# Performance work log

Hardware: AMD Instinct MI355X
Metric: run time of the kernel (lower is better)

The kernel has to match this reference:

```python
import jax, jax.numpy as jnp
import numpy as np

B, C, H, W = 32, 256, 64, 64
MIP, OUP = 8, 256
BN_EPS = 1e-5


def setup_inputs() -> dict:
    key = jax.random.key(0)
    ks = jax.random.split(key, 8)
    x = jax.random.normal(ks[0], (B, C, H, W), dtype=jnp.float32)
    # 1x1 conv weights stored as (out_ch, in_ch); BN in eval mode (running stats)
    w1 = jax.random.normal(ks[1], (MIP, C), dtype=jnp.float32) * 0.05
    bn_gamma = jnp.ones((MIP,), jnp.float32)
    bn_beta = jnp.zeros((MIP,), jnp.float32)
    bn_mean = jax.random.normal(ks[2], (MIP,), dtype=jnp.float32) * 0.1
    bn_var = jax.random.uniform(ks[3], (MIP,), dtype=jnp.float32) + 0.5
    wh = jax.random.normal(ks[4], (OUP, MIP), dtype=jnp.float32) * 0.1
    ww = jax.random.normal(ks[5], (OUP, MIP), dtype=jnp.float32) * 0.1
    return {"x": x, "w1": w1, "bn_gamma": bn_gamma, "bn_beta": bn_beta,
            "bn_mean": bn_mean, "bn_var": bn_var, "wh": wh, "ww": ww}


def _hswish(y):
    return y * jnp.clip(y + 3.0, 0.0, 6.0) / 6.0


def reference(x, w1, bn_gamma, bn_beta, bn_mean, bn_var, wh, ww):
    b, c, h, w = x.shape
    identity = x
    # Shift (mode='max'): pooled softmax profiles, outer product bias map
    bias_h = jax.nn.softmax(jnp.max(x, axis=3, keepdims=True), axis=2)  # (b,c,h,1)
    bias_w = jax.nn.softmax(jnp.max(x, axis=2, keepdims=True), axis=3)  # (b,c,1,w)
    xb = x + bias_h * bias_w  # outer product via broadcast == matmul((h,1),(1,w))
    # avg-pool profiles, concat along spatial axis -> (b,c,h+w,1)
    a_h = jnp.mean(xb, axis=3, keepdims=True)                 # (b,c,h,1)
    a_w = jnp.mean(xb, axis=2, keepdims=True).transpose(0, 1, 3, 2)  # (b,c,w,1)
    y = jnp.concatenate([a_h, a_w], axis=2)                   # (b,c,h+w,1)
    # 1x1 conv -> BN (eval) -> h_swish
    y = jnp.einsum('mc,bcsl->bmsl', w1, y)
    scale = (bn_gamma / jnp.sqrt(bn_var + BN_EPS)).reshape(1, -1, 1, 1)
    shift = (bn_beta - bn_mean * bn_gamma / jnp.sqrt(bn_var + BN_EPS)).reshape(1, -1, 1, 1)
    y = _hswish(y * scale + shift)
    # split, 1x1 convs, sigmoid gates
    y_h, y_w = y[:, :, :h], y[:, :, h:]
    g_h = jax.nn.sigmoid(jnp.einsum('om,bmhl->bohl', wh, y_h))               # (b,oup,h,1)
    g_w = jax.nn.sigmoid(jnp.einsum('om,bmwl->bowl', ww, y_w)).transpose(0, 1, 3, 2)  # (b,oup,1,w)
    return identity * g_w * g_h
```

## Files before the change

kernel.cpp:

```cpp
#include <hip/hip_runtime.h>
#include <math.h>

#define Bn 32
#define Cn 256
#define Hn 64
#define Wn 64
#define MIP 8
#define OUP 256
#define BN_EPS 1e-5f

__global__ __launch_bounds__(256) void stats_kernel(const float* __restrict__ x,
                                                    float* __restrict__ A) {
    const int bc = blockIdx.x;
    const float* xp = x + (size_t)bc * (Hn * Wn);
    __shared__ float tile[Hn * 65];
    const int t = threadIdx.x;

#pragma unroll
    for (int k = 0; k < 4; ++k) {
        int i4  = t + 256 * k;
        int idx = i4 * 4;
        int h = idx >> 6;
        int w = idx & 63;
        float4 v = ((const float4*)xp)[i4];
        float* dst = &tile[h * 65 + w];
        dst[0] = v.x; dst[1] = v.y; dst[2] = v.z; dst[3] = v.w;
    }
    __syncthreads();

    float red_max = -INFINITY, red_sum = 0.f;
    if (t < 64) {
        int h = t;
#pragma unroll 8
        for (int w = 0; w < Wn; ++w) {
            float v = tile[h * 65 + w];
            red_max = fmaxf(red_max, v);
            red_sum += v;
        }
    } else if (t < 128) {
        int w = t - 64;
#pragma unroll 8
        for (int h = 0; h < Hn; ++h) {
            float v = tile[h * 65 + w];
            red_max = fmaxf(red_max, v);
            red_sum += v;
        }
    }

    if (t < 128) {
        float m = red_max;
#pragma unroll
        for (int off = 32; off > 0; off >>= 1) m = fmaxf(m, __shfl_xor(m, off));
        float e = expf(red_max - m);
        float se = e;
#pragma unroll
        for (int off = 32; off > 0; off >>= 1) se += __shfl_xor(se, off);
        float bias = e / se;
        float a = red_sum * (1.0f / 64.0f) + bias * (1.0f / 64.0f);
        A[(size_t)bc * 128 + t] = a;
    }
}

__global__ __launch_bounds__(256) void gates_kernel(const float* __restrict__ A,
                                                    const float* __restrict__ w1,
                                                    const float* __restrict__ bn_gamma,
                                                    const float* __restrict__ bn_beta,
                                                    const float* __restrict__ bn_mean,
                                                    const float* __restrict__ bn_var,
                                                    const float* __restrict__ wh,
                                                    const float* __restrict__ ww,
                                                    float* __restrict__ G) {
    const int b = blockIdx.x;
    const int t = threadIdx.x;
    const int s  = t & 127;
    const int mb = t >> 7;

    const float* Ab = A + (size_t)b * Cn * 128;

    float acc[4] = {0.f, 0.f, 0.f, 0.f};
    for (int c = 0; c < Cn; ++c) {
        float a = Ab[(size_t)c * 128 + s];
#pragma unroll
        for (int k = 0; k < 4; ++k)
            acc[k] += w1[(mb + 2 * k) * Cn + c] * a;
    }

    __shared__ float yact[MIP][128];
#pragma unroll
    for (int k = 0; k < 4; ++k) {
        int m = mb + 2 * k;
        float sc = bn_gamma[m] * rsqrtf(bn_var[m] + BN_EPS);
        float sh = bn_beta[m] - bn_mean[m] * sc;
        float v = acc[k] * sc + sh;
        v = v * fminf(fmaxf(v + 3.0f, 0.0f), 6.0f) * (1.0f / 6.0f);
        yact[m][s] = v;
    }
    __syncthreads();

    float ym[MIP];
#pragma unroll
    for (int m = 0; m < MIP; ++m) ym[m] = yact[m][s];
    const float* w2 = (s < 64) ? wh : ww;

    float* Gb = G + (size_t)b * OUP * 128;
    for (int j = 0; j < 128; ++j) {
        int o = (t >> 7) + 2 * j;
        float g = 0.f;
#pragma unroll
        for (int m = 0; m < MIP; ++m) g += w2[o * MIP + m] * ym[m];
        g = 1.0f / (1.0f + expf(-g));
        Gb[(size_t)o * 128 + s] = g;
    }
}

__global__ __launch_bounds__(256) void apply_kernel(const float* __restrict__ x,
                                                    const float* __restrict__ G,
                                                    float* __restrict__ out) {
    const int bc = blockIdx.x;
    const float* xp = x + (size_t)bc * (Hn * Wn);
    float* op = out + (size_t)bc * (Hn * Wn);
    const float* gp = G + (size_t)bc * 128;

    __shared__ float gs[128];
    const int t = threadIdx.x;
    if (t < 128) gs[t] = gp[t];
    __syncthreads();

#pragma unroll
    for (int k = 0; k < 4; ++k) {
        int i4  = t + 256 * k;
        int idx = i4 * 4;
        int h = idx >> 6;
        int w = idx & 63;
        float4 v = ((const float4*)xp)[i4];
        float gh = gs[h];
        v.x *= gh * gs[64 + w + 0];
        v.y *= gh * gs[64 + w + 1];
        v.z *= gh * gs[64 + w + 2];
        v.w *= gh * gs[64 + w + 3];
        ((float4*)op)[i4] = v;
    }
}

extern "C" void kernel_launch(void* const* d_in, const int* in_sizes, int n_in,
                              void* d_out, int out_size, void* d_ws, size_t ws_size,
                              hipStream_t stream) {
    const float* x        = (const float*)d_in[0];
    const float* w1       = (const float*)d_in[1];
    const float* bn_gamma = (const float*)d_in[2];
    const float* bn_beta  = (const float*)d_in[3];
    const float* bn_mean  = (const float*)d_in[4];
    const float* bn_var   = (const float*)d_in[5];
    const float* wh       = (const float*)d_in[6];
    const float* ww       = (const float*)d_in[7];
    float* out = (float*)d_out;

    float* A = (float*)d_ws;
    float* G = A + (size_t)Bn * Cn * 128;

    stats_kernel<<<Bn * Cn, 256, 0, stream>>>(x, A);
    gates_kernel<<<Bn, 256, 0, stream>>>(A, w1, bn_gamma, bn_beta, bn_mean,
                                         bn_var, wh, ww, G);
    apply_kernel<<<Bn * Cn, 256, 0, stream>>>(x, G, out);
}
```

Measured before the change: 310.6 us.

## Fuse gate computation into apply kernel and split channel reduction in ymix

The second 1x1 conv and sigmoid move out of the 32-block gates kernel into the apply kernel, where each block computes its own 128 gates from the 8-channel activations. This drops the per-batch serial loop over 256 outputs and the G write and read. The remaining ymix kernel splits the 256-channel reduction across the two thread halves and combines them through shared memory. The cost is a small amount of redundant gate arithmetic and extra weight loads in every apply block.

Result: faster. 298.4 us (-3.9%).

```diff
diff --git a/kernel.cpp b/kernel.cpp
--- a/kernel.cpp
+++ b/kernel.cpp
@@ -55,75 +55,78 @@
         float se = e;
 #pragma unroll
         for (int off = 32; off > 0; off >>= 1) se += __shfl_xor(se, off);
-        float bias = e / se;
-        float a = red_sum * (1.0f / 64.0f) + bias * (1.0f / 64.0f);
+        float a = (red_sum + e / se) * (1.0f / 64.0f);
         A[(size_t)bc * 128 + t] = a;
     }
 }
 
-__global__ __launch_bounds__(256) void gates_kernel(const float* __restrict__ A,
-                                                    const float* __restrict__ w1,
-                                                    const float* __restrict__ bn_gamma,
-                                                    const float* __restrict__ bn_beta,
-                                                    const float* __restrict__ bn_mean,
-                                                    const float* __restrict__ bn_var,
-                                                    const float* __restrict__ wh,
-                                                    const float* __restrict__ ww,
-                                                    float* __restrict__ G) {
+__global__ __launch_bounds__(256) void ymix_kernel(const float* __restrict__ A,
+                                                   const float* __restrict__ w1,
+                                                   const float* __restrict__ bn_gamma,
+                                                   const float* __restrict__ bn_beta,
+                                                   const float* __restrict__ bn_mean,
+                                                   const float* __restrict__ bn_var,
+                                                   float* __restrict__ yact) {
     const int b = blockIdx.x;
     const int t = threadIdx.x;
-    const int s  = t & 127;
-    const int mb = t >> 7;
+    const int s    = t & 127;
+    const int half = t >> 7;
 
     const float* Ab = A + (size_t)b * Cn * 128;
 
-    float acc[4] = {0.f, 0.f, 0.f, 0.f};
-    for (int c = 0; c < Cn; ++c) {
+    float acc[MIP];
+#pragma unroll
+    for (int m = 0; m < MIP; ++m) acc[m] = 0.f;
+
+    const int c0 = half * 128;
+    for (int c = c0; c < c0 + 128; ++c) {
         float a = Ab[(size_t)c * 128 + s];
 #pragma unroll
-        for (int k = 0; k < 4; ++k)
-            acc[k] += w1[(mb + 2 * k) * Cn + c] * a;
+        for (int m = 0; m < MIP; ++m)
+            acc[m] += w1[m * Cn + c] * a;
     }
 
-    __shared__ float yact[MIP][128];
+    __shared__ float red[MIP][128];
+    if (half == 1) {
 #pragma unroll
-    for (int k = 0; k < 4; ++k) {
-        int m = mb + 2 * k;
-        float sc = bn_gamma[m] * rsqrtf(bn_var[m] + BN_EPS);
-        float sh = bn_beta[m] - bn_mean[m] * sc;
-        float v = acc[k] * sc + sh;
-        v = v * fminf(fmaxf(v + 3.0f, 0.0f), 6.0f) * (1.0f / 6.0f);
-        yact[m][s] = v;
+        for (int m = 0; m < MIP; ++m) red[m][s] = acc[m];
     }
     __syncthreads();
-
-    float ym[MIP];
+    if (half == 0) {
 #pragma unroll
-    for (int m = 0; m < MIP; ++m) ym[m] = yact[m][s];
-    const float* w2 = (s < 64) ? wh : ww;
-
-    float* Gb = G + (size_t)b * OUP * 128;
-    for (int j = 0; j < 128; ++j) {
-        int o = (t >> 7) + 2 * j;
-        float g = 0.f;
-#pragma unroll
-        for (int m = 0; m < MIP; ++m) g += w2[o * MIP + m] * ym[m];
-        g = 1.0f / (1.0f + expf(-g));
-        Gb[(size_t)o * 128 + s] = g;
+        for (int m = 0; m < MIP; ++m) {
+            float v = acc[m] + red[m][s];
+            float sc = bn_gamma[m] * rsqrtf(bn_var[m] + BN_EPS);
+            float sh = bn_beta[m] - bn_mean[m] * sc;
+            v = v * sc + sh;
+            v = v * fminf(fmaxf(v + 3.0f, 0.0f), 6.0f) * (1.0f / 6.0f);
+            yact[(size_t)b * (MIP * 128) + m * 128 + s] = v;
+        }
     }
 }
 
 __global__ __launch_bounds__(256) void apply_kernel(const float* __restrict__ x,
-                                                    const float* __restrict__ G,
+                                                    const float* __restrict__ yact,
+                                                    const float* __restrict__ wh,
+                                                    const float* __restrict__ ww,
                                                     float* __restrict__ out) {
     const int bc = blockIdx.x;
+    const int b  = bc >> 8;
+    const int c  = bc & 255;
     const float* xp = x + (size_t)bc * (Hn * Wn);
     float* op = out + (size_t)bc * (Hn * Wn);
-    const float* gp = G + (size_t)bc * 128;
 
     __shared__ float gs[128];
     const int t = threadIdx.x;
-    if (t < 128) gs[t] = gp[t];
+    if (t < 128) {
+        const float* w2row = (t < 64) ? (wh + c * MIP) : (ww + c * MIP);
+        const float* yb = yact + (size_t)b * (MIP * 128);
+        float g = 0.f;
+#pragma unroll
+        for (int m = 0; m < MIP; ++m)
+            g += w2row[m] * yb[m * 128 + t];
+        gs[t] = 1.0f / (1.0f + expf(-g));
+    }
     __syncthreads();
 
 #pragma unroll
@@ -155,11 +158,11 @@
     const float* ww       = (const float*)d_in[7];
     float* out = (float*)d_out;
 
-    float* A = (float*)d_ws;
-    float* G = A + (size_t)Bn * Cn * 128;
+    float* A    = (float*)d_ws;
+    float* yact = A + (size_t)Bn * Cn * 128;
 
     stats_kernel<<<Bn * Cn, 256, 0, stream>>>(x, A);
-    gates_kernel<<<Bn, 256, 0, stream>>>(A, w1, bn_gamma, bn_beta, bn_mean,
-                                         bn_var, wh, ww, G);
-    apply_kernel<<<Bn * Cn, 256, 0, stream>>>(x, G, out);
+    ymix_kernel<<<Bn, 256, 0, stream>>>(A, w1, bn_gamma, bn_beta, bn_mean,
+                                        bn_var, yact);
+    apply_kernel<<<Bn * Cn, 256, 0, stream>>>(x, yact, wh, ww, out);
 }
```
